# Optimization experiments

Measured on AMD Instinct MI355X. Metric: run time of the kernel, lower is better.

The kernel has to match this reference:

```python
import jax, jax.numpy as jnp
import numpy as np

K = 3            # kernel_size
KK = K * K       # 9 neighbors per pixel
DILATIONS = [1, 2, 3]
NUM_HEADS = 3


def conv2d(x, w, b, dilation, padding):
    # x: [B,Cin,H,W], w: [Cout,Cin,kh,kw]
    out = jax.lax.conv_general_dilated(
        x, w, window_strides=(1, 1),
        padding=((padding, padding), (padding, padding)),
        rhs_dilation=(dilation, dilation),
        dimension_numbers=('NCHW', 'OIHW', 'NCHW'))
    if b is not None:
        out = out + b[None, :, None, None]
    return out


def unfold3(x, dil):
    # nn.Unfold(kernel=3, dilation=dil, padding=dil, stride=1): [B,C,H,W] -> [B, C*9, H*W]
    B, C, H, W = x.shape
    xp = jnp.pad(x, ((0, 0), (0, 0), (dil, dil), (dil, dil)))
    patches = [xp[:, :, i * dil:i * dil + H, j * dil:j * dil + W]
               for i in range(K) for j in range(K)]
    p = jnp.stack(patches, axis=2)          # [B,C,9,H,W] (channel-major like torch unfold)
    return p.reshape(B, C * KK, H * W)


def bilinear_sample(x, py, px):
    # x: [B,C,H,W]; py, px: [B,K2,H,W] float sample coords -> [B,C,K2,H,W]
    B, C, H, W = x.shape
    K2 = py.shape[1]
    y0 = jnp.floor(py); x0 = jnp.floor(px)
    wy = py - y0; wx = px - x0
    x_flat = x.reshape(B, C, H * W)

    def gather(yi, xi):
        yii = yi.astype(jnp.int32); xii = xi.astype(jnp.int32)
        valid = (yii >= 0) & (yii < H) & (xii >= 0) & (xii < W)
        yc = jnp.clip(yii, 0, H - 1); xc = jnp.clip(xii, 0, W - 1)
        idx = (yc * W + xc).reshape(B, -1)                       # [B, K2*H*W]
        vals = jnp.take_along_axis(x_flat, idx[:, None, :], axis=2)
        vals = vals.reshape(B, C, K2, H, W)
        return vals * valid[:, None].astype(x.dtype)

    v00 = gather(y0, x0); v01 = gather(y0, x0 + 1)
    v10 = gather(y0 + 1, x0); v11 = gather(y0 + 1, x0 + 1)
    wy = wy[:, None]; wx = wx[:, None]
    return (v00 * (1 - wy) * (1 - wx) + v01 * (1 - wy) * wx
            + v10 * wy * (1 - wx) + v11 * wy * wx)


def deform_conv(x, offsets, w, b, dil):
    # torchvision DeformConv2d, stride 1, padding=dil, dilation=dil, kernel 3
    B, C, H, W = x.shape
    off = offsets.reshape(B, KK, 2, H, W)                 # [..., (dy,dx), ...]
    ky, kx = jnp.meshgrid(jnp.arange(K), jnp.arange(K), indexing='ij')
    base_dy = (ky.reshape(KK) * dil - dil).astype(x.dtype)
    base_dx = (kx.reshape(KK) * dil - dil).astype(x.dtype)
    hh = jnp.arange(H, dtype=x.dtype); ww = jnp.arange(W, dtype=x.dtype)
    py = hh[None, None, :, None] + base_dy[None, :, None, None] + off[:, :, 0]
    px = ww[None, None, None, :] + base_dx[None, :, None, None] + off[:, :, 1]
    sampled = bilinear_sample(x, py, px)                  # [B,C,9,H,W]
    out = jnp.einsum('bckhw,ock->bohw', sampled, w.reshape(w.shape[0], C, KK))
    return out + b[None, :, None, None]


def adda_attention(q, k, v, head_dim, dil, deform_params):
    # q,k,v: [B,d,H,W] (already stop-gradiented)
    B, d, H, W = q.shape
    scale = head_dim ** -0.5
    if dil != 1:
        ow, ob, dw, db = deform_params
        offsets = conv2d(k, ow, ob, dil, dil)             # [B, 2*9, H, W]
        k = deform_conv(k, offsets, dw, db, dil)
        v = deform_conv(v, offsets, dw, db, dil)
    ku = unfold3(k, dil)                                  # [B, d*9, HW]
    vu = unfold3(v, dil)
    g = d // head_dim
    HW = H * W
    qh = q.reshape(B, g, head_dim, 1, HW).transpose(0, 1, 4, 3, 2)   # [B,g,HW,1,hd]
    kh = ku.reshape(B, g, head_dim, KK, HW).transpose(0, 1, 4, 2, 3) # [B,g,HW,hd,9]
    vh = vu.reshape(B, g, head_dim, KK, HW).transpose(0, 1, 4, 3, 2) # [B,g,HW,9,hd]
    attn = jax.nn.softmax((qh @ kh) * scale, axis=-1)                # [B,g,HW,1,9]
    o = attn @ vh                                                    # [B,g,HW,1,hd]
    return o.transpose(0, 2, 1, 3, 4).reshape(B, H, W, d)


def setup_inputs() -> dict:
    key = jax.random.key(0)
    ks = jax.random.split(key, 16)
    B, H, W, C = 8, 64, 64, 192
    hd = C // NUM_HEADS  # 64 == C // num_dilation
    inp = {
        'x': jax.random.normal(ks[0], (B, H, W, C), jnp.float32),
        'qkv_w': jax.random.normal(ks[1], (3 * C, C, 1, 1), jnp.float32) * 0.05,
        'proj_w': jax.random.normal(ks[2], (C, C), jnp.float32) * 0.05,
        'proj_b': jnp.zeros((C,), jnp.float32),
        'off_w2': jax.random.normal(ks[3], (2 * KK, hd, K, K), jnp.float32) * 0.01,
        'off_b2': jnp.zeros((2 * KK,), jnp.float32),
        'def_w2': jax.random.normal(ks[4], (hd, hd, K, K), jnp.float32) * 0.05,
        'def_b2': jnp.zeros((hd,), jnp.float32),
        'off_w3': jax.random.normal(ks[5], (2 * KK, hd, K, K), jnp.float32) * 0.01,
        'off_b3': jnp.zeros((2 * KK,), jnp.float32),
        'def_w3': jax.random.normal(ks[6], (hd, hd, K, K), jnp.float32) * 0.05,
        'def_b3': jnp.zeros((hd,), jnp.float32),
    }
    return inp


def reference(x, qkv_w, proj_w, proj_b,
              off_w2, off_b2, def_w2, def_b2,
              off_w3, off_b3, def_w3, def_b3):
    B, H, W, C = x.shape
    nd = len(DILATIONS)
    d = C // nd
    hd = C // NUM_HEADS
    xc = x.transpose(0, 3, 1, 2)                              # [B,C,H,W]
    qkv = conv2d(xc, qkv_w, None, 1, 0)                       # [B,3C,H,W]
    qkv = qkv.reshape(B, 3, nd, d, H, W).transpose(2, 1, 0, 3, 4, 5)  # [nd,3,B,d,H,W]
    qkv = jax.lax.stop_gradient(qkv)                          # q,k,v are .detach()'d in torch
    deform = {2: (off_w2, off_b2, def_w2, def_b2),
              3: (off_w3, off_b3, def_w3, def_b3)}
    outs = []
    for i, dil in enumerate(DILATIONS):
        outs.append(adda_attention(qkv[i, 0], qkv[i, 1], qkv[i, 2],
                                   hd, dil, deform.get(dil)))
    out = jnp.stack(outs, axis=3).reshape(B, H, W, C)         # permute(1,2,3,0,4).reshape
    return out @ proj_w.T + proj_b
```

## Files before the change

### kernel.cpp

```cpp
#include <hip/hip_runtime.h>
#include <cmath>

#define kB    8
#define kH    64
#define kW    64
#define kHW   4096
#define kC    192
#define kD    64
#define kM    (kB * kHW)
#define kNQKV 576

typedef unsigned short ushort_t;
typedef __attribute__((ext_vector_type(8))) short  s8v;
typedef __attribute__((ext_vector_type(4))) float  f4v;

__device__ inline unsigned short bf16r(float f) {
    union { float f; unsigned u; } v; v.f = f;
    unsigned u = v.u + 0x7FFFu + ((v.u >> 16) & 1u);
    return (unsigned short)(u >> 16);
}
__device__ inline float bfu(short s) {
    union { unsigned u; float f; } v;
    v.u = ((unsigned)(unsigned short)s) << 16;
    return v.f;
}

__global__ void cvt_prep(const float* __restrict__ x, unsigned* __restrict__ xb,
                         const float* __restrict__ qkv_w,
                         const float* __restrict__ proj_w,
                         const float* __restrict__ def_w2,
                         const float* __restrict__ def_w3,
                         const float* __restrict__ off_w2,
                         const float* __restrict__ off_w3,
                         ushort_t* __restrict__ awb,
                         ushort_t* __restrict__ pwbp,
                         ushort_t* __restrict__ dwtb2,
                         ushort_t* __restrict__ dwtb3,
                         ushort_t* __restrict__ owtb2,
                         ushort_t* __restrict__ owtb3) {
    const int bid = blockIdx.x;
    const int tid = threadIdx.x;
    if (bid < 12288) {
        int i = bid * 256 + tid;
        if (i >= kM * kC / 2) return;
        float2 f = ((const float2*)x)[i];
        xb[i] = (unsigned)bf16r(f.x) | ((unsigned)bf16r(f.y) << 16);
    } else if (bid < 12342) {
        int idx = (bid - 12288) * 256 + tid;
        if (idx >= 36 * 6 * 64) return;
        int lane = idx & 63;
        int kc   = (idx >> 6) % 6;
        int s    = idx / 384;
        int row  = s * 16 + (lane & 15);
        int k0   = kc * 32 + (lane >> 4) * 8;
        const float* src = qkv_w + (size_t)row * kC + k0;
        ushort_t* dst = awb + (size_t)idx * 8;
#pragma unroll
        for (int j = 0; j < 8; ++j) dst[j] = bf16r(src[j]);
    } else if (bid < 12360) {
        int idx = (bid - 12342) * 256 + tid;
        if (idx >= 12 * 6 * 64) return;
        int lane = idx & 63;
        int kc   = (idx >> 6) % 6;
        int s    = idx / 384;
        int row  = s * 16 + (lane & 15);
        int k0   = kc * 32 + (lane >> 4) * 8;
        const float* src = proj_w + (size_t)row * kC + k0;
        ushort_t* dst = pwbp + (size_t)idx * 8;
#pragma unroll
        for (int j = 0; j < 8; ++j) dst[j] = bf16r(src[j]);
    } else if (bid < 12648) {
        const float* dw = (bid < 12504) ? def_w2 : def_w3;
        ushort_t* dwtb  = (bid < 12504) ? dwtb2 : dwtb3;
        int l = ((bid < 12504) ? (bid - 12360) : (bid - 12504)) * 256 + tid;
        if (l >= kD * kD * 9) return;
        int o = l / 576;
        int c = (l / 9) % 64;
        int kk = l % 9;
        dwtb[(kk * 64 + o) * 64 + c] = bf16r(dw[l]);
    } else {
        const float* ow = (bid < 12720) ? off_w2 : off_w3;
        ushort_t* owtb  = (bid < 12720) ? owtb2 : owtb3;
        int l = ((bid < 12720) ? (bid - 12648) : (bid - 12720)) * 256 + tid;
        if (l >= 9 * 32 * 64) return;
        int kk = l >> 11;
        int j  = (l >> 6) & 31;
        int c  = l & 63;
        owtb[l] = (j < 18) ? bf16r(ow[j * 576 + c * 9 + kk]) : (ushort_t)0;
    }
}

__global__ __launch_bounds__(256) void qkv_mfma3(const ushort_t* __restrict__ xb,
                                                 const ushort_t* __restrict__ awb,
                                                 ushort_t* __restrict__ qkvpx) {
    __shared__ ushort_t xs[64 * kC];

    const int tid = threadIdx.x;
    const int bx  = blockIdx.x;
    const int lb  = (bx & 7) * 64 + (bx >> 3);
    const int m0  = lb * 64;
    const int ty3 = blockIdx.y;

#pragma unroll
    for (int i = 0; i < 6; ++i) {
        int il = i * 256 + tid;
        int p  = il / 24;
        int cc = il % 24;
        uint4 v = *(const uint4*)(xb + (size_t)(m0 + p) * kC + cc * 8);
        int dst = p * 384 + ((cc * 16) ^ ((p & 7) << 4));
        *(uint4*)((char*)xs + dst) = v;
    }
    __syncthreads();

    const int lane = tid & 63;
    const int wave = tid >> 6;
    const int l15  = lane & 15;
    const int q    = lane >> 4;
    const int sbase = ty3 * 12 + wave * 3;

    f4v acc[3][4];
#pragma unroll
    for (int i = 0; i < 3; ++i)
#pragma unroll
        for (int m = 0; m < 4; ++m) acc[i][m] = (f4v){0.f, 0.f, 0.f, 0.f};

    const ushort_t* ap = awb + ((size_t)sbase * 6 * 64 + lane) * 8;

#pragma unroll
    for (int kc = 0; kc < 6; ++kc) {
        s8v bfr[4];
#pragma unroll
        for (int m = 0; m < 4; ++m) {
            int row = m * 16 + l15;
            int col = (kc * 64 + q * 16) ^ ((l15 & 7) << 4);
            bfr[m] = *(const s8v*)((const char*)xs + row * 384 + col);
        }
#pragma unroll
        for (int i = 0; i < 3; ++i) {
            s8v a = *(const s8v*)(ap + (size_t)(i * 6 + kc) * 64 * 8);
#pragma unroll
            for (int m = 0; m < 4; ++m)
                acc[i][m] = __builtin_amdgcn_mfma_f32_16x16x32_bf16(a, bfr[m], acc[i][m], 0, 0, 0);
        }
    }

#pragma unroll
    for (int i = 0; i < 3; ++i) {
        int s   = sbase + i;
        int ty  = s >> 2;
        int c64 = (s & 3) * 16 + q * 4;
        ushort_t* obase = qkvpx + (size_t)ty * kM * 64 + (size_t)m0 * 64 + c64;
#pragma unroll
        for (int m = 0; m < 4; ++m) {
            f4v v = acc[i][m];
            uint2 u;
            u.x = (unsigned)bf16r(v.x) | ((unsigned)bf16r(v.y) << 16);
            u.y = (unsigned)bf16r(v.z) | ((unsigned)bf16r(v.w) << 16);
            *(uint2*)(obase + (size_t)(m * 16 + l15) * 64) = u;
        }
    }
}

__global__ __launch_bounds__(256) void off_conv_fused(const ushort_t* __restrict__ k1,
                                                      const ushort_t* __restrict__ k2,
                                                      const ushort_t* __restrict__ owtb2,
                                                      const ushort_t* __restrict__ owtb3,
                                                      const float* __restrict__ ob2,
                                                      const float* __restrict__ ob3,
                                                      float* __restrict__ offb2,
                                                      float* __restrict__ offb3) {
    const int bx = blockIdx.x;
    const int lb = (bx & 7) * 128 + (bx >> 3);
    const int zb = lb >> 9;
    const int rest = lb & 511;
    const int b = rest >> 6;
    const int y = rest & 63;
    const int dil = 2 + zb;
    const ushort_t* kpx  = zb ? k2 : k1;
    const ushort_t* owtb = zb ? owtb3 : owtb2;
    const float* obias   = zb ? ob3 : ob2;
    float* offb          = zb ? offb3 : offb2;

    const int tid  = threadIdx.x;
    const int lane = tid & 63;
    const int wave = tid >> 6;
    const int l15  = lane & 15;
    const int q    = lane >> 4;
    const int px   = wave * 16 + l15;

    const ushort_t* inpx = kpx + (size_t)b * kHW * 64 + q * 8;

    f4v acc[2];
    acc[0] = (f4v){0.f, 0.f, 0.f, 0.f};
    acc[1] = (f4v){0.f, 0.f, 0.f, 0.f};

#pragma unroll
    for (int kk = 0; kk < 9; ++kk) {
        const int yy = y + (kk / 3 - 1) * dil;
        const int xx = px + (kk % 3 - 1) * dil;
        const bool valid = (yy >= 0) & (yy < kH) & (xx >= 0) & (xx < kW);
        const size_t idx = valid ? (size_t)(yy * kW + xx) * 64 : 0;
        s8v a0 = *(const s8v*)(inpx + idx);
        s8v a1 = *(const s8v*)(inpx + idx + 32);
        if (!valid) {
            a0 = (s8v){0, 0, 0, 0, 0, 0, 0, 0};
            a1 = (s8v){0, 0, 0, 0, 0, 0, 0, 0};
        }
        const ushort_t* wb = owtb + (size_t)kk * 2048 + l15 * 64 + q * 8;
#pragma unroll
        for (int nbk = 0; nbk < 2; ++nbk) {
            s8v b0 = *(const s8v*)(wb + nbk * 1024);
            s8v b1 = *(const s8v*)(wb + nbk * 1024 + 32);
            acc[nbk] = __builtin_amdgcn_mfma_f32_16x16x32_bf16(a0, b0, acc[nbk], 0, 0, 0);
            acc[nbk] = __builtin_amdgcn_mfma_f32_16x16x32_bf16(a1, b1, acc[nbk], 0, 0, 0);
        }
    }
#pragma unroll
    for (int nbk = 0; nbk < 2; ++nbk) {
        int n = nbk * 16 + l15;
        if (n < 18) {
            float bias = obias[n];
            f4v v = acc[nbk];
            v.x += bias; v.y += bias; v.z += bias; v.w += bias;
            *(f4v*)&offb[((size_t)b * 18 + n) * kHW + y * kW + wave * 16 + q * 4] = v;
        }
    }
}

__global__ __launch_bounds__(1024) void deform_big(const ushort_t* __restrict__ k1,
                                                   const ushort_t* __restrict__ v1,
                                                   const ushort_t* __restrict__ k2,
                                                   const ushort_t* __restrict__ v2,
                                                   const float* __restrict__ offb2,
                                                   const float* __restrict__ offb3,
                                                   const ushort_t* __restrict__ dwtb2,
                                                   const ushort_t* __restrict__ dwtb3,
                                                   const float* __restrict__ db2,
                                                   const float* __restrict__ db3,
                                                   ushort_t* __restrict__ kd2,
                                                   ushort_t* __restrict__ vd2,
                                                   ushort_t* __restrict__ kd3,
                                                   ushort_t* __restrict__ vd3) {
    __shared__ ushort_t kv[12 * 4096];
    __shared__ ushort_t wlds[5 * 4096];

    const int tid = threadIdx.x;
    const int bx  = blockIdx.x;
    const int lb  = (bx & 7) * 64 + (bx >> 3);
    const int zb  = lb >> 8;
    const int t   = (lb >> 7) & 1;
    const int b   = (lb >> 4) & 7;
    const int y0  = (lb & 15) * 4;
    const int dil = 2 + zb;
    const int nr  = 2 * dil + 6;
    const int wlo = y0 - dil - 1;

    const ushort_t* kin = zb ? k2 : k1;
    const ushort_t* vin = zb ? v2 : v1;
    const float* offbS  = zb ? offb3 : offb2;
    const ushort_t* dwtb = zb ? dwtb3 : dwtb2;
    const float* db      = zb ? db3 : db2;
    ushort_t* outp = t ? (zb ? vd3 : vd2) : (zb ? kd3 : kd2);

    const ushort_t* inb = (t ? vin : kin) + (size_t)b * kHW * 64;

    {
        int half  = tid >> 9;
        int chunk = tid & 511;
        int xcol  = chunk >> 3;
        int cc    = chunk & 7;
        int dstc  = (xcol * 128 + cc * 16) ^ ((xcol & 7) << 4);
        for (int r0 = 0; r0 < nr; r0 += 2) {
            int r = r0 + half;
            if (r < nr) {
                int gy = min(max(wlo + r, 0), kH - 1);
                *(uint4*)((char*)kv + r * 8192 + dstc) =
                    *(const uint4*)(inb + (size_t)gy * 4096 + chunk * 8);
            }
        }
    }
    for (int i = tid; i < 2560; i += 1024) {
        int g = i * 16;
        uint4 v = *(const uint4*)((const char*)dwtb + g);
        int row = (g >> 7) & 63;
        *(uint4*)((char*)wlds + (g ^ ((row & 7) << 4))) = v;
    }
    __syncthreads();

    const int lane = tid & 63;
    const int wave = tid >> 6;
    const int ry   = wave >> 2;
    const int wc   = wave & 3;
    const int l15  = lane & 15;
    const int q    = lane >> 4;
    const int y    = y0 + ry;
    const int px   = wc * 16 + l15;
    const int wsw  = (l15 & 7) << 4;
    const int wcol0 = (q * 16) ^ wsw;
    const int wcol1 = (q * 16 + 64) ^ wsw;

    const ushort_t* inpx = inb + q * 8;

    f4v acc[4];
#pragma unroll
    for (int ob = 0; ob < 4; ++ob) acc[ob] = (f4v){0.f, 0.f, 0.f, 0.f};

    const float* offrow = offbS + (size_t)b * 18 * kHW + y * kW + px;
    float offv[18];
#pragma unroll
    for (int i = 0; i < 18; ++i) offv[i] = offrow[(size_t)i * kHW];

    auto do_tap = [&](int kk, int kkbase) {
        float oy = offv[kk * 2 + 0];
        float ox = offv[kk * 2 + 1];
        float py  = (float)y  + (float)((kk / 3 - 1) * dil) + oy;
        float pxf = (float)px + (float)((kk % 3 - 1) * dil) + ox;
        float fy = floorf(py), fx = floorf(pxf);
        float wy = py - fy, wx = pxf - fx;
        int iy0 = (int)fy, ix0 = (int)fx;
        int iy1 = iy0 + 1, ix1 = ix0 + 1;
        int y0c = min(max(iy0, 0), kH - 1), x0c = min(max(ix0, 0), kW - 1);
        int y1c = min(max(iy1, 0), kH - 1), x1c = min(max(ix1, 0), kW - 1);
        bool vy0 = (iy0 >= 0) & (iy0 < kH), vx0 = (ix0 >= 0) & (ix0 < kW);
        bool vy1 = (iy1 >= 0) & (iy1 < kH), vx1 = (ix1 >= 0) & (ix1 < kW);
        float w0 = (vy0 && vx0) ? (1.f - wy) * (1.f - wx) : 0.f;
        float w1 = (vy0 && vx1) ? (1.f - wy) * wx : 0.f;
        float w2 = (vy1 && vx0) ? wy * (1.f - wx) : 0.f;
        float w3 = (vy1 && vx1) ? wy * wx : 0.f;

        s8v c[8];
        if (__builtin_expect(fabsf(oy) < 1.0f, 1)) {
            int r0 = min(max(y0c - wlo, 0), nr - 1);
            int r1 = min(max(y1c - wlo, 0), nr - 1);
            int b00 = r0 * 8192 + ((x0c * 128 + q * 16) ^ ((x0c & 7) << 4));
            int b00h = r0 * 8192 + ((x0c * 128 + q * 16 + 64) ^ ((x0c & 7) << 4));
            int b01 = r0 * 8192 + ((x1c * 128 + q * 16) ^ ((x1c & 7) << 4));
            int b01h = r0 * 8192 + ((x1c * 128 + q * 16 + 64) ^ ((x1c & 7) << 4));
            int b10 = r1 * 8192 + ((x0c * 128 + q * 16) ^ ((x0c & 7) << 4));
            int b10h = r1 * 8192 + ((x0c * 128 + q * 16 + 64) ^ ((x0c & 7) << 4));
            int b11 = r1 * 8192 + ((x1c * 128 + q * 16) ^ ((x1c & 7) << 4));
            int b11h = r1 * 8192 + ((x1c * 128 + q * 16 + 64) ^ ((x1c & 7) << 4));
            c[0] = *(const s8v*)((const char*)kv + b00);
            c[1] = *(const s8v*)((const char*)kv + b00h);
            c[2] = *(const s8v*)((const char*)kv + b01);
            c[3] = *(const s8v*)((const char*)kv + b01h);
            c[4] = *(const s8v*)((const char*)kv + b10);
            c[5] = *(const s8v*)((const char*)kv + b10h);
            c[6] = *(const s8v*)((const char*)kv + b11);
            c[7] = *(const s8v*)((const char*)kv + b11h);
        } else {
            size_t i00 = (size_t)(y0c * kW + x0c) * 64;
            size_t i01 = (size_t)(y0c * kW + x1c) * 64;
            size_t i10 = (size_t)(y1c * kW + x0c) * 64;
            size_t i11 = (size_t)(y1c * kW + x1c) * 64;
            c[0] = *(const s8v*)(inpx + i00);
            c[1] = *(const s8v*)(inpx + i00 + 32);
            c[2] = *(const s8v*)(inpx + i01);
            c[3] = *(const s8v*)(inpx + i01 + 32);
            c[4] = *(const s8v*)(inpx + i10);
            c[5] = *(const s8v*)(inpx + i10 + 32);
            c[6] = *(const s8v*)(inpx + i11);
            c[7] = *(const s8v*)(inpx + i11 + 32);
        }

        s8v b0, b1;
#pragma unroll
        for (int j = 0; j < 8; ++j) {
            float v0 = w0 * bfu(c[0][j]) + w1 * bfu(c[2][j]) +
                       w2 * bfu(c[4][j]) + w3 * bfu(c[6][j]);
            float v1 = w0 * bfu(c[1][j]) + w1 * bfu(c[3][j]) +
                       w2 * bfu(c[5][j]) + w3 * bfu(c[7][j]);
            b0[j] = (short)bf16r(v0);
            b1[j] = (short)bf16r(v1);
        }
        const char* wkk = (const char*)wlds + (kk - kkbase) * 8192 + l15 * 128;
#pragma unroll
        for (int obb = 0; obb < 4; ++obb) {
            s8v a0w = *(const s8v*)(wkk + obb * 2048 + wcol0);
            s8v a1w = *(const s8v*)(wkk + obb * 2048 + wcol1);
            acc[obb] = __builtin_amdgcn_mfma_f32_16x16x32_bf16(a0w, b0, acc[obb], 0, 0, 0);
            acc[obb] = __builtin_amdgcn_mfma_f32_16x16x32_bf16(a1w, b1, acc[obb], 0, 0, 0);
        }
    };

#pragma unroll
    for (int kk = 0; kk < 5; ++kk) do_tap(kk, 0);
    __syncthreads();
    for (int i = tid; i < 2048; i += 1024) {
        int g = i * 16;
        uint4 v = *(const uint4*)((const char*)dwtb + 40960 + g);
        int row = (g >> 7) & 63;
        *(uint4*)((char*)wlds + (g ^ ((row & 7) << 4))) = v;
    }
    __syncthreads();
#pragma unroll
    for (int kk = 5; kk < 9; ++kk) do_tap(kk, 5);

    ushort_t* orow = outp + ((size_t)b * kHW + y * kW + px) * 64 + q * 4;
#pragma unroll
    for (int obb = 0; obb < 4; ++obb) {
        float4 bias = *(const float4*)&db[obb * 16 + q * 4];
        f4v v = acc[obb];
        uint2 u;
        u.x = (unsigned)bf16r(v.x + bias.x) | ((unsigned)bf16r(v.y + bias.y) << 16);
        u.y = (unsigned)bf16r(v.z + bias.z) | ((unsigned)bf16r(v.w + bias.w) << 16);
        *(uint2*)(orow + obb * 16) = u;
    }
}

__global__ __launch_bounds__(512) void attn_fused(const ushort_t* __restrict__ q0,
                                                  const ushort_t* __restrict__ k0,
                                                  const ushort_t* __restrict__ v0,
                                                  const ushort_t* __restrict__ q1,
                                                  const ushort_t* __restrict__ kd2,
                                                  const ushort_t* __restrict__ vd2,
                                                  const ushort_t* __restrict__ q2,
                                                  const ushort_t* __restrict__ kd3,
                                                  const ushort_t* __restrict__ vd3,
                                                  ushort_t* __restrict__ aopx) {
    __shared__ ushort_t ks[8 * 4096];
    __shared__ ushort_t vs[8 * 4096];

    const int tid = threadIdx.x;
    const int bx  = blockIdx.x;
    const int lb  = (bx & 7) * 96 + (bx >> 3);
    const int zb  = lb >> 8;
    const int rest = lb & 255;
    const int b   = rest >> 5;
    const int y0  = (rest & 31) * 2;
    const int dil = zb + 1;
    const int nr  = 2 * dil + 2;
    const int wlo = y0 - dil;

    const ushort_t* qpx = (zb == 0) ? q0 : (zb == 1) ? q1 : q2;
    const ushort_t* kpx = (zb == 0) ? k0 : (zb == 1) ? kd2 : kd3;
    const ushort_t* vpx = (zb == 0) ? v0 : (zb == 1) ? vd2 : vd3;

    const size_t pbase = (size_t)b * kHW;
    const ushort_t* kb = kpx + pbase * 64;
    const ushort_t* vb = vpx + pbase * 64;

    {
        int x  = tid >> 3;
        int cc = tid & 7;
        int dstc = (x * 128 + cc * 16) ^ ((x & 7) << 4);
        for (int r = 0; r < nr; ++r) {
            int gy = min(max(wlo + r, 0), kH - 1);
            *(uint4*)((char*)ks + r * 8192 + dstc) = *(const uint4*)(kb + (size_t)gy * 4096 + tid * 8);
            *(uint4*)((char*)vs + r * 8192 + dstc) = *(const uint4*)(vb + (size_t)gy * 4096 + tid * 8);
        }
    }
    __syncthreads();

    const int wave = tid >> 6;
    const int l    = tid & 63;
    const int ry   = wave >> 2;
    const int wc   = wave & 3;
    const int pxq  = l >> 2;
    const int cg   = l & 3;
    const int y  = y0 + ry;
    const int x_ = wc * 16 + pxq;
    const int p  = y * kW + x_;

    const ushort_t* qb = qpx + (pbase + p) * 64 + cg * 16;
    s8v qv0 = *(const s8v*)qb;
    s8v qv1 = *(const s8v*)(qb + 8);
    float qf[16];
#pragma unroll
    for (int j = 0; j < 8; ++j) { qf[j] = bfu(qv0[j]); qf[8 + j] = bfu(qv1[j]); }

    int a0s[9], a1s[9];
    float msk[9];
#pragma unroll
    for (int kk = 0; kk < 9; ++kk) {
        int dy = (kk / 3 - 1) * dil, dx = (kk % 3 - 1) * dil;
        int yy = y + dy, xx = x_ + dx;
        bool v = (yy >= 0) & (yy < kH) & (xx >= 0) & (xx < kW);
        msk[kk] = v ? 1.f : 0.f;
        int r  = min(max(yy - wlo, 0), nr - 1);
        int xc = min(max(xx, 0), kW - 1);
        int sw = (xc & 7) << 4;
        a0s[kk] = r * 8192 + ((xc * 128 + cg * 32) ^ sw);
        a1s[kk] = r * 8192 + ((xc * 128 + cg * 32 + 16) ^ sw);
    }

    float e[9];
#pragma unroll
    for (int kk = 0; kk < 9; ++kk) {
        s8v k0v = *(const s8v*)((const char*)ks + a0s[kk]);
        s8v k1v = *(const s8v*)((const char*)ks + a1s[kk]);
        float s = 0.f;
#pragma unroll
        for (int j = 0; j < 8; ++j) {
            s += qf[j] * bfu(k0v[j]);
            s += qf[8 + j] * bfu(k1v[j]);
        }
        s += __shfl_xor(s, 1);
        s += __shfl_xor(s, 2);
        e[kk] = s * 0.125f * msk[kk];
    }
    float mx = -1e30f;
#pragma unroll
    for (int kk = 0; kk < 9; ++kk) mx = fmaxf(mx, e[kk]);
    float ssum = 0.f;
#pragma unroll
    for (int kk = 0; kk < 9; ++kk) { e[kk] = __expf(e[kk] - mx); ssum += e[kk]; }
    float inv = 1.f / ssum;
#pragma unroll
    for (int kk = 0; kk < 9; ++kk) e[kk] = e[kk] * inv * msk[kk];

    float acc[16];
#pragma unroll
    for (int j = 0; j < 16; ++j) acc[j] = 0.f;
#pragma unroll
    for (int kk = 0; kk < 9; ++kk) {
        s8v v0v = *(const s8v*)((const char*)vs + a0s[kk]);
        s8v v1v = *(const s8v*)((const char*)vs + a1s[kk]);
        float w = e[kk];
#pragma unroll
        for (int j = 0; j < 8; ++j) {
            acc[j] += w * bfu(v0v[j]);
            acc[8 + j] += w * bfu(v1v[j]);
        }
    }
    unsigned u[8];
#pragma unroll
    for (int i = 0; i < 8; ++i)
        u[i] = (unsigned)bf16r(acc[2 * i]) | ((unsigned)bf16r(acc[2 * i + 1]) << 16);
    ushort_t* ob = aopx + (pbase + p) * kC + zb * 64 + cg * 16;
    *(uint4*)ob = make_uint4(u[0], u[1], u[2], u[3]);
    *(uint4*)(ob + 8) = make_uint4(u[4], u[5], u[6], u[7]);
}

__global__ __launch_bounds__(256) void proj_mfma3(const ushort_t* __restrict__ aopx,
                                                  const ushort_t* __restrict__ pwbp,
                                                  const float* __restrict__ pb,
                                                  float* __restrict__ out) {
    __shared__ ushort_t xs[64 * kC];

    const int tid = threadIdx.x;
    const int bx  = blockIdx.x;
    const int lb  = (bx & 7) * 64 + (bx >> 3);
    const int m0  = lb * 64;

#pragma unroll
    for (int i = 0; i < 6; ++i) {
        int il = i * 256 + tid;
        int p  = il / 24;
        int cc = il % 24;
        uint4 v = *(const uint4*)(aopx + (size_t)(m0 + p) * kC + cc * 8);
        int dst = p * 384 + ((cc * 16) ^ ((p & 7) << 4));
        *(uint4*)((char*)xs + dst) = v;
    }
    __syncthreads();

    const int lane = tid & 63;
    const int wave = tid >> 6;
    const int l15  = lane & 15;
    const int q    = lane >> 4;
    const int sbase = wave * 3;

    f4v acc[3][4];
#pragma unroll
    for (int i = 0; i < 3; ++i)
#pragma unroll
        for (int m = 0; m < 4; ++m) acc[i][m] = (f4v){0.f, 0.f, 0.f, 0.f};

    const ushort_t* ap = pwbp + ((size_t)sbase * 6 * 64 + lane) * 8;

#pragma unroll
    for (int kc = 0; kc < 6; ++kc) {
        s8v bfr[4];
#pragma unroll
        for (int m = 0; m < 4; ++m) {
            int row = m * 16 + l15;
            int col = (kc * 64 + q * 16) ^ ((l15 & 7) << 4);
            bfr[m] = *(const s8v*)((const char*)xs + row * 384 + col);
        }
#pragma unroll
        for (int i = 0; i < 3; ++i) {
            s8v a = *(const s8v*)(ap + (size_t)(i * 6 + kc) * 64 * 8);
#pragma unroll
            for (int m = 0; m < 4; ++m)
                acc[i][m] = __builtin_amdgcn_mfma_f32_16x16x32_bf16(a, bfr[m], acc[i][m], 0, 0, 0);
        }
    }

#pragma unroll
    for (int i = 0; i < 3; ++i) {
        int s  = sbase + i;
        int n0 = s * 16 + q * 4;
        float4 bias = *(const float4*)&pb[n0];
#pragma unroll
        for (int m = 0; m < 4; ++m) {
            f4v v = acc[i][m];
            v.x += bias.x; v.y += bias.y; v.z += bias.z; v.w += bias.w;
            *(f4v*)&out[(size_t)(m0 + m * 16 + l15) * kC + n0] = v;
        }
    }
}

extern "C" void kernel_launch(void* const* d_in, const int* in_sizes, int n_in,
                              void* d_out, int out_size, void* d_ws, size_t ws_size,
                              hipStream_t stream) {
    const float* x      = (const float*)d_in[0];
    const float* qkv_w  = (const float*)d_in[1];
    const float* proj_w = (const float*)d_in[2];
    const float* proj_b = (const float*)d_in[3];
    const float* off_w2 = (const float*)d_in[4];
    const float* off_b2 = (const float*)d_in[5];
    const float* def_w2 = (const float*)d_in[6];
    const float* def_b2 = (const float*)d_in[7];
    const float* off_w3 = (const float*)d_in[8];
    const float* off_b3 = (const float*)d_in[9];
    const float* def_w3 = (const float*)d_in[10];
    const float* def_b3 = (const float*)d_in[11];
    float* out = (float*)d_out;

    float* ws    = (float*)d_ws;
    float* offb2 = ws;
    float* offb3 = offb2 + (size_t)18 * kM;
    ushort_t* us = (ushort_t*)(offb3 + (size_t)18 * kM);
    ushort_t* xb     = us;  us += (size_t)kM * kC;
    ushort_t* qkvpx  = us;  us += (size_t)9 * kM * 64;
    ushort_t* kd2    = us;  us += (size_t)kM * 64;
    ushort_t* vd2    = us;  us += (size_t)kM * 64;
    ushort_t* kd3    = us;  us += (size_t)kM * 64;
    ushort_t* vd3    = us;  us += (size_t)kM * 64;
    ushort_t* aopx   = us;  us += (size_t)kM * kC;
    ushort_t* awb    = us;  us += (size_t)kNQKV * kC;
    ushort_t* pwbp   = us;  us += (size_t)kC * kC;
    ushort_t* dwtb2  = us;  us += kD * kD * 9;
    ushort_t* dwtb3  = us;  us += kD * kD * 9;
    ushort_t* owtb2  = us;  us += 9 * 32 * 64;
    ushort_t* owtb3  = us;  us += 9 * 32 * 64;

    cvt_prep<<<12792, 256, 0, stream>>>(x, (unsigned*)xb, qkv_w, proj_w,
                                        def_w2, def_w3, off_w2, off_w3,
                                        awb, pwbp, dwtb2, dwtb3, owtb2, owtb3);

    ushort_t* q0 = qkvpx;
    ushort_t* q1 = qkvpx + (size_t)1 * kM * 64;
    ushort_t* q2 = qkvpx + (size_t)2 * kM * 64;
    ushort_t* k0 = qkvpx + (size_t)3 * kM * 64;
    ushort_t* k1 = qkvpx + (size_t)4 * kM * 64;
    ushort_t* k2 = qkvpx + (size_t)5 * kM * 64;
    ushort_t* v0 = qkvpx + (size_t)6 * kM * 64;
    ushort_t* v1 = qkvpx + (size_t)7 * kM * 64;
    ushort_t* v2 = qkvpx + (size_t)8 * kM * 64;

    qkv_mfma3<<<dim3(kM / 64, 3), 256, 0, stream>>>(xb, awb, qkvpx);

    off_conv_fused<<<1024, 256, 0, stream>>>(k1, k2, owtb2, owtb3,
                                             off_b2, off_b3, offb2, offb3);

    deform_big<<<512, 1024, 0, stream>>>(k1, v1, k2, v2, offb2, offb3,
                                         dwtb2, dwtb3, def_b2, def_b3,
                                         kd2, vd2, kd3, vd3);

    attn_fused<<<768, 512, 0, stream>>>(q0, k0, v0, q1, kd2, vd2, q2, kd3, vd3, aopx);

    proj_mfma3<<<512, 256, 0, stream>>>(aopx, pwbp, proj_b, out);
}
```

Baseline: 209.9 us.

## Stage offset-conv inputs in LDS, pack bilinear math, share attention K/V buffer

```diff
diff --git a/kernel.cpp b/kernel.cpp
--- a/kernel.cpp
+++ b/kernel.cpp
@@ -13,6 +13,7 @@
 typedef unsigned short ushort_t;
 typedef __attribute__((ext_vector_type(8))) short  s8v;
 typedef __attribute__((ext_vector_type(4))) float  f4v;
+typedef __attribute__((ext_vector_type(2))) float  f2v;
 
 __device__ inline unsigned short bf16r(float f) {
     union { float f; unsigned u; } v; v.f = f;
@@ -23,6 +24,19 @@
     union { unsigned u; float f; } v;
     v.u = ((unsigned)(unsigned short)s) << 16;
     return v.f;
+}
+__device__ inline f2v bfu2(unsigned u) {
+    union { unsigned u; float f; } lo, hi;
+    lo.u = u << 16;
+    hi.u = u & 0xFFFF0000u;
+    return (f2v){lo.f, hi.f};
+}
+__device__ inline unsigned pk2(f2v a) {
+    union { float f; unsigned u; } x, y;
+    x.f = a.x; y.f = a.y;
+    unsigned ua = x.u + 0x7FFFu + ((x.u >> 16) & 1u);
+    unsigned ub = y.u + 0x7FFFu + ((y.u >> 16) & 1u);
+    return (ua >> 16) | (ub & 0xFFFF0000u);
 }
 
 __global__ void cvt_prep(const float* __restrict__ x, unsigned* __restrict__ xb,
@@ -169,6 +183,8 @@
                                                       const float* __restrict__ ob3,
                                                       float* __restrict__ offb2,
                                                       float* __restrict__ offb3) {
+    __shared__ ushort_t ks[7 * 4096];
+
     const int bx = blockIdx.x;
     const int lb = (bx & 7) * 128 + (bx >> 3);
     const int zb = lb >> 9;
@@ -176,20 +192,35 @@
     const int b = rest >> 6;
     const int y = rest & 63;
     const int dil = 2 + zb;
+    const int nr  = 2 * dil + 1;
+    const int wlo = y - dil;
     const ushort_t* kpx  = zb ? k2 : k1;
     const ushort_t* owtb = zb ? owtb3 : owtb2;
     const float* obias   = zb ? ob3 : ob2;
     float* offb          = zb ? offb3 : offb2;
 
     const int tid  = threadIdx.x;
+    const ushort_t* kb = kpx + (size_t)b * kHW * 64;
+
+    for (int r = 0; r < nr; ++r) {
+        int gy = min(max(wlo + r, 0), kH - 1);
+#pragma unroll
+        for (int h = 0; h < 2; ++h) {
+            int chunk = h * 256 + tid;
+            int xcol = chunk >> 3, cc = chunk & 7;
+            int dstc = (xcol * 128 + cc * 16) ^ ((xcol & 7) << 4);
+            *(uint4*)((char*)ks + r * 8192 + dstc) =
+                *(const uint4*)(kb + (size_t)gy * 4096 + chunk * 8);
+        }
+    }
+    __syncthreads();
+
     const int lane = tid & 63;
     const int wave = tid >> 6;
     const int l15  = lane & 15;
     const int q    = lane >> 4;
     const int px   = wave * 16 + l15;
 
-    const ushort_t* inpx = kpx + (size_t)b * kHW * 64 + q * 8;
-
     f4v acc[2];
     acc[0] = (f4v){0.f, 0.f, 0.f, 0.f};
     acc[1] = (f4v){0.f, 0.f, 0.f, 0.f};
@@ -199,9 +230,11 @@
         const int yy = y + (kk / 3 - 1) * dil;
         const int xx = px + (kk % 3 - 1) * dil;
         const bool valid = (yy >= 0) & (yy < kH) & (xx >= 0) & (xx < kW);
-        const size_t idx = valid ? (size_t)(yy * kW + xx) * 64 : 0;
-        s8v a0 = *(const s8v*)(inpx + idx);
-        s8v a1 = *(const s8v*)(inpx + idx + 32);
+        int r  = min(max(yy - wlo, 0), nr - 1);
+        int xc = min(max(xx, 0), kW - 1);
+        int sw = (xc & 7) << 4;
+        s8v a0 = *(const s8v*)((const char*)ks + r * 8192 + ((xc * 128 + q * 16) ^ sw));
+        s8v a1 = *(const s8v*)((const char*)ks + r * 8192 + ((xc * 128 + q * 16 + 64) ^ sw));
         if (!valid) {
             a0 = (s8v){0, 0, 0, 0, 0, 0, 0, 0};
             a1 = (s8v){0, 0, 0, 0, 0, 0, 0, 0};
@@ -363,15 +396,20 @@
             c[7] = *(const s8v*)(inpx + i11 + 32);
         }
 
+        const f2v w0v = {w0, w0}, w1v = {w1, w1}, w2v = {w2, w2}, w3v = {w3, w3};
         s8v b0, b1;
 #pragma unroll
-        for (int j = 0; j < 8; ++j) {
-            float v0 = w0 * bfu(c[0][j]) + w1 * bfu(c[2][j]) +
-                       w2 * bfu(c[4][j]) + w3 * bfu(c[6][j]);
-            float v1 = w0 * bfu(c[1][j]) + w1 * bfu(c[3][j]) +
-                       w2 * bfu(c[5][j]) + w3 * bfu(c[7][j]);
-            b0[j] = (short)bf16r(v0);
-            b1[j] = (short)bf16r(v1);
+        for (int jp = 0; jp < 4; ++jp) {
+            f2v a0 = w0v * bfu2(((const unsigned*)&c[0])[jp])
+                   + w1v * bfu2(((const unsigned*)&c[2])[jp])
+                   + w2v * bfu2(((const unsigned*)&c[4])[jp])
+                   + w3v * bfu2(((const unsigned*)&c[6])[jp]);
+            f2v a1 = w0v * bfu2(((const unsigned*)&c[1])[jp])
+                   + w1v * bfu2(((const unsigned*)&c[3])[jp])
+                   + w2v * bfu2(((const unsigned*)&c[5])[jp])
+                   + w3v * bfu2(((const unsigned*)&c[7])[jp]);
+            ((unsigned*)&b0)[jp] = pk2(a0);
+            ((unsigned*)&b1)[jp] = pk2(a1);
         }
         const char* wkk = (const char*)wlds + (kk - kkbase) * 8192 + l15 * 128;
 #pragma unroll
@@ -418,8 +456,7 @@
                                                   const ushort_t* __restrict__ kd3,
                                                   const ushort_t* __restrict__ vd3,
                                                   ushort_t* __restrict__ aopx) {
-    __shared__ ushort_t ks[8 * 4096];
-    __shared__ ushort_t vs[8 * 4096];
+    __shared__ ushort_t kvs[8 * 4096];
 
     const int tid = threadIdx.x;
     const int bx  = blockIdx.x;
@@ -440,15 +477,13 @@
     const ushort_t* kb = kpx + pbase * 64;
     const ushort_t* vb = vpx + pbase * 64;
 
-    {
-        int x  = tid >> 3;
-        int cc = tid & 7;
-        int dstc = (x * 128 + cc * 16) ^ ((x & 7) << 4);
-        for (int r = 0; r < nr; ++r) {
-            int gy = min(max(wlo + r, 0), kH - 1);
-            *(uint4*)((char*)ks + r * 8192 + dstc) = *(const uint4*)(kb + (size_t)gy * 4096 + tid * 8);
-            *(uint4*)((char*)vs + r * 8192 + dstc) = *(const uint4*)(vb + (size_t)gy * 4096 + tid * 8);
-        }
+    const int stx  = tid >> 3;
+    const int stcc = tid & 7;
+    const int dstc = (stx * 128 + stcc * 16) ^ ((stx & 7) << 4);
+
+    for (int r = 0; r < nr; ++r) {
+        int gy = min(max(wlo + r, 0), kH - 1);
+        *(uint4*)((char*)kvs + r * 8192 + dstc) = *(const uint4*)(kb + (size_t)gy * 4096 + tid * 8);
     }
     __syncthreads();
 
@@ -487,8 +522,8 @@
     float e[9];
 #pragma unroll
     for (int kk = 0; kk < 9; ++kk) {
-        s8v k0v = *(const s8v*)((const char*)ks + a0s[kk]);
-        s8v k1v = *(const s8v*)((const char*)ks + a1s[kk]);
+        s8v k0v = *(const s8v*)((const char*)kvs + a0s[kk]);
+        s8v k1v = *(const s8v*)((const char*)kvs + a1s[kk]);
         float s = 0.f;
 #pragma unroll
         for (int j = 0; j < 8; ++j) {
@@ -509,13 +544,20 @@
 #pragma unroll
     for (int kk = 0; kk < 9; ++kk) e[kk] = e[kk] * inv * msk[kk];
 
+    __syncthreads();
+    for (int r = 0; r < nr; ++r) {
+        int gy = min(max(wlo + r, 0), kH - 1);
+        *(uint4*)((char*)kvs + r * 8192 + dstc) = *(const uint4*)(vb + (size_t)gy * 4096 + tid * 8);
+    }
+    __syncthreads();
+
     float acc[16];
 #pragma unroll
     for (int j = 0; j < 16; ++j) acc[j] = 0.f;
 #pragma unroll
     for (int kk = 0; kk < 9; ++kk) {
-        s8v v0v = *(const s8v*)((const char*)vs + a0s[kk]);
-        s8v v1v = *(const s8v*)((const char*)vs + a1s[kk]);
+        s8v v0v = *(const s8v*)((const char*)kvs + a0s[kk]);
+        s8v v1v = *(const s8v*)((const char*)kvs + a1s[kk]);
         float w = e[kk];
 #pragma unroll
         for (int j = 0; j < 8; ++j) {
```

Result: faster. 204.6 us (-2.5%).
